# Kernel optimization log

Measured on AMD Instinct MI355X. Metric: run time of the kernel, lower is better.

The kernel has to match this reference:

```python
import jax, jax.numpy as jnp
import numpy as np
from jax import lax

B, H, W, CIN = 4, 64, 64, 1024
CMID = 512
NA = 9  # 3 sizes * 3 ratios
PRE_NMS, POST_NMS, IOU_THR = 6000, 300, 0.7  # eval-mode caps (training=False)


def setup_inputs() -> dict:
    key = jax.random.key(0)
    ks = jax.random.split(key, 4)
    feats = jax.random.normal(ks[0], (B, H, W, CIN), jnp.float32)
    # anchors: normalized ccwh (cx, cy, w, h) on a stride-16 grid of a 1024px image
    stride, img = 16.0, 1024.0
    cx = (jnp.arange(W, dtype=jnp.float32) + 0.5) * stride / img
    cy = (jnp.arange(H, dtype=jnp.float32) + 0.5) * stride / img
    sizes = jnp.array([64.0, 128.0, 256.0])
    ratios = jnp.array([0.5, 1.0, 2.0])
    ws = (sizes[:, None] * jnp.sqrt(ratios)[None, :]).reshape(-1) / img  # [9]
    hs = (sizes[:, None] / jnp.sqrt(ratios)[None, :]).reshape(-1) / img  # [9]
    cyg, cxg = jnp.meshgrid(cy, cx, indexing='ij')  # [H,W]
    ancs = jnp.stack([
        jnp.broadcast_to(cxg[:, :, None], (H, W, NA)),
        jnp.broadcast_to(cyg[:, :, None], (H, W, NA)),
        jnp.broadcast_to(ws[None, None, :], (H, W, NA)),
        jnp.broadcast_to(hs[None, None, :], (H, W, NA)),
    ], axis=-1)
    ancs = jnp.broadcast_to(ancs[None], (B, H, W, NA, 4)).astype(jnp.float32)
    ancs_valid = jnp.ones((B, H, W, NA), jnp.float32)
    w_bneck = jax.random.normal(ks[1], (CIN, CMID), jnp.float32) * 0.01
    b_bneck = jnp.zeros((CMID,), jnp.float32)
    w_cls = jax.random.normal(ks[2], (CMID, NA), jnp.float32) * 0.01
    b_cls = jnp.zeros((NA,), jnp.float32)
    w_reg = jax.random.normal(ks[3], (CMID, NA * 4), jnp.float32) * 0.01
    b_reg = jnp.zeros((NA * 4,), jnp.float32)
    return dict(feats=feats, ancs=ancs, ancs_valid=ancs_valid,
                w_bneck=w_bneck, b_bneck=b_bneck, w_cls=w_cls, b_cls=b_cls,
                w_reg=w_reg, b_reg=b_reg)


def _nms(boxes, max_out, thr):
    # boxes [N,4] xyxy, sorted by score descending. Greedy NMS via lax.scan.
    x1, y1, x2, y2 = boxes[:, 0], boxes[:, 1], boxes[:, 2], boxes[:, 3]
    areas = (x2 - x1) * (y2 - y1)

    def step(valid, _):
        idx = jnp.argmax(valid)  # first still-valid box = highest score
        has = valid[idx]
        b = boxes[idx]
        a = areas[idx]
        iw = jnp.maximum(jnp.minimum(b[2], x2) - jnp.maximum(b[0], x1), 0.0)
        ih = jnp.maximum(jnp.minimum(b[3], y2) - jnp.maximum(b[1], y1), 0.0)
        inter = iw * ih
        union = a + areas - inter
        iou = jnp.where(union > 0, inter / union, 0.0)
        keep = valid & (iou <= thr)
        keep = keep.at[idx].set(False)
        return jnp.where(has, keep, valid), jnp.where(has, idx, -1)

    _, sel = lax.scan(step, jnp.ones(boxes.shape[0], bool), None, length=max_out)
    return sel  # [max_out] selected indices, -1 = no more boxes


def _forward(feats, ancs, w_bneck, b_bneck, w_cls, b_cls, w_reg, b_reg):
    h = jax.nn.relu(jnp.einsum('bhwc,cm->bhwm', feats, w_bneck) + b_bneck)
    cls_pred = jax.nn.sigmoid(jnp.einsum('bhwm,mo->bhwo', h, w_cls) + b_cls)
    reg_pred = (jnp.einsum('bhwm,mo->bhwo', h, w_reg) + b_reg).reshape(B, H, W, NA, 4)
    cls_f = cls_pred.reshape(-1)
    reg_f = reg_pred.reshape(-1, 4)
    anc_f = ancs.reshape(-1, 4)
    # apply_offsets in ccwh: cx += tx*w, cy += ty*h, w *= exp(tw), h *= exp(th)
    cx = anc_f[:, 0] + reg_f[:, 0] * anc_f[:, 2]
    cy = anc_f[:, 1] + reg_f[:, 1] * anc_f[:, 3]
    ww = anc_f[:, 2] * jnp.exp(reg_f[:, 2])
    hh = anc_f[:, 3] * jnp.exp(reg_f[:, 3])
    # ccwh -> xyxy, clip to [0,1]
    boxes = jnp.stack([cx - ww / 2, cy - hh / 2, cx + ww / 2, cy + hh / 2], axis=-1)
    boxes = jnp.clip(boxes, 0.0, 1.0)
    order = jnp.argsort(-cls_f)[:PRE_NMS]
    boxes = boxes[order]
    sel = _nms(boxes, POST_NMS, IOU_THR)
    # pad unselected slots with zeros (TF returns a variable-length tensor)
    proposals = jnp.where(sel[:, None] >= 0, boxes[jnp.clip(sel, 0)], 0.0)
    return cls_pred, reg_pred, proposals


def reference(feats, ancs, ancs_valid, w_bneck, b_bneck, w_cls, b_cls, w_reg, b_reg):
    # ancs_valid is reshaped but never used in the original extract_proposals
    return _forward(feats, ancs, w_bneck, b_bneck, w_cls, b_cls, w_reg, b_reg)
```

## Files before the change

### kernel.cpp

```cpp
#include <hip/hip_runtime.h>
#include <cstdint>
#include <cstddef>

#define P_TOT    16384
#define CIN      1024
#define CMID     512
#define NA       9
#define NANC     147456
#define PRE_NMS  6000
#define POST_NMS 300
#define IOU_THR  0.7f
#define NWORDS   94
#define NHCOPY   4

#define CLS_OFF  0
#define REG_OFF  147456
#define PROP_OFF 737280

#define WS_H        0u
#define WS_MASK     0u
#define WS_HISTN    33554432u
#define WS_WCOMBT   34603008u
#define WS_BOXES    36700160u
#define WS_HIST     39059456u
#define WS_META     39321600u
#define WS_COLL     39321856u
#define WS_SBOX     39387392u
#define CAP_COLL    8192

__device__ __forceinline__ int imin(int a, int b) { return a < b ? a : b; }

__device__ __forceinline__ void gld_lds16f(const float* g, float* l) {
    __builtin_amdgcn_global_load_lds(
        (const __attribute__((address_space(1))) void*)g,
        (__attribute__((address_space(3))) void*)l,
        16, 0, 0);
}

__global__ __launch_bounds__(256)
__attribute__((amdgpu_waves_per_eu(1, 2)))
void gemm1_kernel(
    const float* __restrict__ A, const float* __restrict__ Bw,
    const float* __restrict__ bias, float* __restrict__ C,
    unsigned int* __restrict__ histN, unsigned int* __restrict__ meta,
    const float* __restrict__ wcls, const float* __restrict__ wreg,
    float* __restrict__ wcombT)
{
    __shared__ float As[2][16][132];
    __shared__ float Bs[2][16][128];

    const int t  = threadIdx.x;

    {
        const int fb = (int)blockIdx.x * 4 + (int)blockIdx.y;
        if (t < 128) {
            uint4* hz = (uint4*)histN;
            hz[fb * 128 + t] = make_uint4(0u, 0u, 0u, 0u);
        }
        if (fb == 0 && t < 64) meta[t] = 0u;
        if (t < 48) {
            float v = 0.f;
            if (t < 9)       v = wcls[fb * 9 + t];
            else if (t < 45) v = wreg[fb * 36 + (t - 9)];
            wcombT[t * CMID + fb] = v;
        }
    }

    const int m0 = blockIdx.x * 128;
    const int n0 = blockIdx.y * 128;
    const int tx = t & 15;
    const int ty = t >> 4;

    const int ar0 = t >> 2;
    const int ac0 = (t & 3) * 4;

    const float* asrc0 = A + (size_t)(m0 + ar0) * CIN + ac0;
    const float* asrc1 = asrc0 + (size_t)64 * CIN;
    const float* bsrc  = Bw + (size_t)(t >> 5) * CMID + n0 + (t & 31) * 4;
    float* bdst0 = &Bs[0][0][0] + t * 4;
    float* bdst1 = &Bs[1][0][0] + t * 4;

    float4 c0a{0,0,0,0}, c0b{0,0,0,0}, c1a{0,0,0,0}, c1b{0,0,0,0};
    float4 c2a{0,0,0,0}, c2b{0,0,0,0}, c3a{0,0,0,0}, c3b{0,0,0,0};
    float4 c4a{0,0,0,0}, c4b{0,0,0,0}, c5a{0,0,0,0}, c5b{0,0,0,0};
    float4 c6a{0,0,0,0}, c6b{0,0,0,0}, c7a{0,0,0,0}, c7b{0,0,0,0};

    gld_lds16f(bsrc, bdst0);
    gld_lds16f(bsrc + 8 * CMID, bdst0 + 1024);
    float4 pa0 = *(const float4*)(asrc0);
    float4 pa1 = *(const float4*)(asrc1);
    As[0][ac0 + 0][ar0] = pa0.x; As[0][ac0 + 1][ar0] = pa0.y;
    As[0][ac0 + 2][ar0] = pa0.z; As[0][ac0 + 3][ar0] = pa0.w;
    As[0][ac0 + 0][ar0 + 64] = pa1.x; As[0][ac0 + 1][ar0 + 64] = pa1.y;
    As[0][ac0 + 2][ar0 + 64] = pa1.z; As[0][ac0 + 3][ar0 + 64] = pa1.w;
    __syncthreads();

#define FMA4(acc, s, b) { acc.x += (s)*(b).x; acc.y += (s)*(b).y; \
                          acc.z += (s)*(b).z; acc.w += (s)*(b).w; }

    for (int kt = 0; kt < 64; ++kt) {
        const int cur = kt & 1, nxt = cur ^ 1;
        if (kt < 63) {
            const int k0 = (kt + 1) * 16;
            float* bd = nxt ? bdst1 : bdst0;
            gld_lds16f(bsrc + (size_t)k0 * CMID, bd);
            gld_lds16f(bsrc + (size_t)(k0 + 8) * CMID, bd + 1024);
            pa0 = *(const float4*)(asrc0 + k0);
            pa1 = *(const float4*)(asrc1 + k0);
        }
#pragma unroll 2
        for (int kk = 0; kk < 16; ++kk) {
            float4 a0 = *(const float4*)&As[cur][kk][ty * 4];
            float4 a1 = *(const float4*)&As[cur][kk][64 + ty * 4];
            float4 b0 = *(const float4*)&Bs[cur][kk][tx * 4];
            float4 b1 = *(const float4*)&Bs[cur][kk][64 + tx * 4];
            FMA4(c0a, a0.x, b0) FMA4(c0b, a0.x, b1)
            FMA4(c1a, a0.y, b0) FMA4(c1b, a0.y, b1)
            FMA4(c2a, a0.z, b0) FMA4(c2b, a0.z, b1)
            FMA4(c3a, a0.w, b0) FMA4(c3b, a0.w, b1)
            FMA4(c4a, a1.x, b0) FMA4(c4b, a1.x, b1)
            FMA4(c5a, a1.y, b0) FMA4(c5b, a1.y, b1)
            FMA4(c6a, a1.z, b0) FMA4(c6b, a1.z, b1)
            FMA4(c7a, a1.w, b0) FMA4(c7b, a1.w, b1)
        }
        if (kt < 63) {
            As[nxt][ac0 + 0][ar0] = pa0.x; As[nxt][ac0 + 1][ar0] = pa0.y;
            As[nxt][ac0 + 2][ar0] = pa0.z; As[nxt][ac0 + 3][ar0] = pa0.w;
            As[nxt][ac0 + 0][ar0 + 64] = pa1.x; As[nxt][ac0 + 1][ar0 + 64] = pa1.y;
            As[nxt][ac0 + 2][ar0 + 64] = pa1.z; As[nxt][ac0 + 3][ar0 + 64] = pa1.w;
        }
        __syncthreads();
    }
#undef FMA4

    const float4 bias0 = *(const float4*)(bias + n0 + tx * 4);
    const float4 bias1 = *(const float4*)(bias + n0 + 64 + tx * 4);
#define STROW(row, ca, cb) { \
    float4 o; \
    o.x = fmaxf(ca.x + bias0.x, 0.f); o.y = fmaxf(ca.y + bias0.y, 0.f); \
    o.z = fmaxf(ca.z + bias0.z, 0.f); o.w = fmaxf(ca.w + bias0.w, 0.f); \
    *(float4*)(C + (size_t)(row) * CMID + n0 + tx * 4) = o; \
    o.x = fmaxf(cb.x + bias1.x, 0.f); o.y = fmaxf(cb.y + bias1.y, 0.f); \
    o.z = fmaxf(cb.z + bias1.z, 0.f); o.w = fmaxf(cb.w + bias1.w, 0.f); \
    *(float4*)(C + (size_t)(row) * CMID + n0 + 64 + tx * 4) = o; }

    const int mr = m0 + ty * 4;
    STROW(mr + 0, c0a, c0b)   STROW(mr + 1, c1a, c1b)
    STROW(mr + 2, c2a, c2b)   STROW(mr + 3, c3a, c3b)
    STROW(mr + 64, c4a, c4b)  STROW(mr + 65, c5a, c5b)
    STROW(mr + 66, c6a, c6b)  STROW(mr + 67, c7a, c7b)
#undef STROW
}

__global__ __launch_bounds__(256) void gemm2_kernel(
    const float* __restrict__ h, const float* __restrict__ wcombT,
    const float* __restrict__ bcls, const float* __restrict__ breg,
    const float4* __restrict__ ancs, float* __restrict__ out,
    float4* __restrict__ boxes, unsigned int* __restrict__ histN)
{
    __shared__ float hS[32][68];
    __shared__ float wT[48][64];
    __shared__ float lt[32][49];

    const int t  = threadIdx.x;
    const int p0 = blockIdx.x * 32;
    const int px = t & 31;
    const int og = t >> 5;

    const int hr = t >> 3;
    const int hc = (t & 7) * 8;

    float acc[6] = {};

    for (int kt = 0; kt < 8; ++kt) {
        const int k0 = kt * 64;
        {
            const float* hp = h + (size_t)(p0 + hr) * CMID + k0 + hc;
            float4 v0 = *(const float4*)(hp);
            float4 v1 = *(const float4*)(hp + 4);
            *(float4*)&hS[hr][hc]     = v0;
            *(float4*)&hS[hr][hc + 4] = v1;
        }
        {
#pragma unroll
            for (int r = 0; r < 3; ++r) {
                int idx = t + r * 256;
                int row = idx >> 4, c4 = (idx & 15) * 4;
                *(float4*)&wT[row][c4] =
                    *(const float4*)&wcombT[(size_t)row * CMID + k0 + c4];
            }
        }
        __syncthreads();
#pragma unroll
        for (int q = 0; q < 16; ++q) {
            float4 hv4 = *(const float4*)&hS[px][q * 4];
            float4 w0 = *(const float4*)&wT[og * 6 + 0][q * 4];
            float4 w1 = *(const float4*)&wT[og * 6 + 1][q * 4];
            float4 w2 = *(const float4*)&wT[og * 6 + 2][q * 4];
            float4 w3 = *(const float4*)&wT[og * 6 + 3][q * 4];
            float4 w4 = *(const float4*)&wT[og * 6 + 4][q * 4];
            float4 w5 = *(const float4*)&wT[og * 6 + 5][q * 4];
            const float* hv = (const float*)&hv4;
            const float* p0w = (const float*)&w0;
            const float* p1w = (const float*)&w1;
            const float* p2w = (const float*)&w2;
            const float* p3w = (const float*)&w3;
            const float* p4w = (const float*)&w4;
            const float* p5w = (const float*)&w5;
#pragma unroll
            for (int j = 0; j < 4; ++j) {
                float hvj = hv[j];
                acc[0] += hvj * p0w[j];
                acc[1] += hvj * p1w[j];
                acc[2] += hvj * p2w[j];
                acc[3] += hvj * p3w[j];
                acc[4] += hvj * p4w[j];
                acc[5] += hvj * p5w[j];
            }
        }
        __syncthreads();
    }

#pragma unroll
    for (int c = 0; c < 6; ++c) {
        int o = og * 6 + c;
        float v = 0.f;
        if (o < 45) {
            float bv = (o < 9) ? bcls[o] : breg[o - 9];
            v = acc[c] + bv;
        }
        lt[px][o] = v;
    }
    __syncthreads();

#pragma unroll
    for (int rr = 0; rr < 2; ++rr) {
        int a_lin = t + rr * 256;
        if (a_lin < 288) {
            int px_l = a_lin / 9;
            int a    = a_lin - px_l * 9;
            int i    = (p0 + px_l) * 9 + a;

            float lg = lt[px_l][a];
            float score = 1.f / (1.f + expf(-lg));
            out[CLS_OFF + i] = score;

            float r0 = lt[px_l][9 + a * 4 + 0];
            float r1 = lt[px_l][9 + a * 4 + 1];
            float r2 = lt[px_l][9 + a * 4 + 2];
            float r3 = lt[px_l][9 + a * 4 + 3];
            float4 rg; rg.x = r0; rg.y = r1; rg.z = r2; rg.w = r3;
            *(float4*)(out + REG_OFF + (size_t)i * 4) = rg;

            float4 an = ancs[i];
            float cx = an.x + r0 * an.z;
            float cy = an.y + r1 * an.w;
            float ww = an.z * expf(r2);
            float hh = an.w * expf(r3);
            float4 bb;
            bb.x = fminf(fmaxf(cx - ww * 0.5f, 0.f), 1.f);
            bb.y = fminf(fmaxf(cy - hh * 0.5f, 0.f), 1.f);
            bb.z = fminf(fmaxf(cx + ww * 0.5f, 0.f), 1.f);
            bb.w = fminf(fmaxf(cy + hh * 0.5f, 0.f), 1.f);
            boxes[i] = bb;

            unsigned int sb = __float_as_uint(score);
            atomicAdd(&histN[(unsigned)(blockIdx.x & (NHCOPY - 1)) * 65536u + (sb >> 16)], 1u);
        }
    }
}

__global__ __launch_bounds__(256) void hreduce_kernel(
    const unsigned int* __restrict__ histN, unsigned int* __restrict__ hist)
{
    int b = blockIdx.x * 256 + threadIdx.x;
    unsigned int s = 0;
#pragma unroll
    for (int c = 0; c < NHCOPY; ++c) s += histN[(unsigned)c * 65536u + b];
    hist[b] = s;
}

__global__ __launch_bounds__(256) void scan_kernel(
    const unsigned int* __restrict__ hist, unsigned int* __restrict__ meta)
{
    __shared__ unsigned int sums[256];
    __shared__ unsigned int sc[256];
    __shared__ unsigned int sc2[256];
    __shared__ int cstar;
    __shared__ unsigned int saShared;
    __shared__ int tbin;

    int t = threadIdx.x;
    if (t == 0) tbin = -1;

    unsigned int s = 0;
    int base = t << 8;
    for (int b = 0; b < 256; b += 4) {
        uint4 v = *(const uint4*)(hist + base + b);
        s += v.x + v.y + v.z + v.w;
    }
    sums[t] = s;
    __syncthreads();

    sc[t] = sums[255 - t];
    __syncthreads();
    for (int off = 1; off < 256; off <<= 1) {
        unsigned int v = sc[t];
        unsigned int add = (t >= off) ? sc[t - off] : 0u;
        __syncthreads();
        sc[t] = v + add;
        __syncthreads();
    }
    {
        unsigned int sa = (t == 255) ? 0u : sc[254 - t];
        if (sa < PRE_NMS && sa + sums[t] >= PRE_NMS) { cstar = t; saShared = sa; }
    }
    __syncthreads();

    int c = cstar;
    unsigned int SA = saShared;
    sc2[t] = hist[c * 256 + 255 - t];
    __syncthreads();
    for (int off = 1; off < 256; off <<= 1) {
        unsigned int v = sc2[t];
        unsigned int add = (t >= off) ? sc2[t - off] : 0u;
        __syncthreads();
        sc2[t] = v + add;
        __syncthreads();
    }
    {
        unsigned int si = sc2[255 - t];
        int cand = (SA + si >= PRE_NMS) ? t : -1;
        atomicMax(&tbin, cand);
    }
    __syncthreads();
    if (t == 0) meta[1] = (unsigned int)(c * 256 + tbin);
}

__global__ __launch_bounds__(256) void collect_kernel(
    const float* __restrict__ scores, const unsigned int* __restrict__ meta,
    unsigned long long* __restrict__ coll, unsigned int* __restrict__ cnt)
{
    int i = blockIdx.x * 256 + threadIdx.x;
    unsigned int T = meta[1];
    unsigned int sb = __float_as_uint(scores[i]);
    if ((sb >> 16) >= T) {
        unsigned int pos = atomicAdd(cnt, 1u);
        if (pos < CAP_COLL)
            coll[pos] = ((unsigned long long)sb << 32) |
                        (unsigned long long)(0xFFFFFFFFu - (unsigned int)i);
    }
}

__global__ __launch_bounds__(256) void rank_kernel(
    const unsigned long long* __restrict__ coll,
    const unsigned int* __restrict__ cnt,
    const float4* __restrict__ boxes, float4* __restrict__ sboxes)
{
    const int t = threadIdx.x;
    const int lane = t & 63;
    const int gwave = blockIdx.x * 4 + (t >> 6);
    unsigned int n = cnt[0];
    if (n > CAP_COLL) n = CAP_COLL;
    if (gwave * 16 >= (int)n) return;

    unsigned long long me[16];
    int rank[16];
#pragma unroll
    for (int i = 0; i < 16; ++i) {
        int mi = gwave * 16 + i;
        me[i] = (mi < (int)n) ? coll[mi] : ~0ULL;
        rank[i] = 0;
    }

    for (int j = 0; j < CAP_COLL; j += 64) {
        unsigned long long k = ((unsigned)(j + lane) < n) ? coll[j + lane] : 0ULL;
#pragma unroll
        for (int i = 0; i < 16; ++i)
            rank[i] += (int)__popcll(__ballot(k > me[i]));
    }

#pragma unroll
    for (int i = 0; i < 16; ++i) {
        int mi = gwave * 16 + i;
        if (mi < (int)n && rank[i] < PRE_NMS && lane == i) {
            unsigned int idx = 0xFFFFFFFFu - (unsigned int)(me[i] & 0xFFFFFFFFULL);
            if (idx > NANC - 1) idx = NANC - 1;
            sboxes[rank[i]] = boxes[idx];
        }
    }
}

__global__ __launch_bounds__(64) void nmsmat_kernel(
    const float4* __restrict__ sboxes, unsigned long long* __restrict__ mask)
{
    const int rb = blockIdx.x, cb = blockIdx.y;
    if (cb < rb) return;
    __shared__ float cx1[64], cy1[64], cx2[64], cy2[64], car[64];

    const int t = threadIdx.x;
    const int c = cb * 64 + t;
    float4 b = (c < PRE_NMS) ? sboxes[c] : make_float4(0.f, 0.f, 0.f, 0.f);
    cx1[t] = b.x; cy1[t] = b.y; cx2[t] = b.z; cy2[t] = b.w;
    car[t] = (b.z - b.x) * (b.w - b.y);
    __syncthreads();

    const int r = rb * 64 + t;
    if (r >= PRE_NMS) return;
    const float4 rbx = sboxes[r];
    const float ra = (rbx.z - rbx.x) * (rbx.w - rbx.y);

    unsigned long long w = 0ULL;
#pragma unroll 8
    for (int i = 0; i < 64; ++i) {
        int j = cb * 64 + i;
        float iw = fmaxf(fminf(rbx.z, cx2[i]) - fmaxf(rbx.x, cx1[i]), 0.f);
        float ih = fmaxf(fminf(rbx.w, cy2[i]) - fmaxf(rbx.y, cy1[i]), 0.f);
        float inter = iw * ih;
        float uni = ra + car[i] - inter;
        float iou = (uni > 0.f) ? (inter / uni) : 0.f;
        if (iou > IOU_THR && j > r) w |= (1ULL << i);
    }
    mask[(size_t)r * NWORDS + cb] = w;
}

__global__ __launch_bounds__(64) void nmsresolve_kernel(
    const float4* __restrict__ sboxes,
    const unsigned long long* __restrict__ mask,
    float* __restrict__ prop)
{
    __shared__ unsigned long long rowbuf[64 * NWORDS];
    __shared__ int picks[POST_NMS];

    const int t = threadIdx.x;
    for (int j = t; j < POST_NMS * 4; j += 64) prop[j] = 0.f;

    const int w0 = 2 * t, w1 = 2 * t + 1;
    unsigned long long s0 = 0ULL, s1 = 0ULL;
    int cnt = 0;

    for (int c = 0; c < NWORDS && cnt < POST_NMS; ++c) {
        unsigned long long aw = __shfl((c & 1) ? s1 : s0, c >> 1, 64);
        unsigned long long valid = ~aw;
        if (c == 93) valid &= (1ULL << 48) - 1ULL;
        if (!valid) continue;

        {
            const float* src = (const float*)(mask + (size_t)c * 64 * NWORDS) + t * 4;
            float* dst = (float*)&rowbuf[0] + t * 4;
#pragma unroll
            for (int k = 0; k < 47; ++k)
                gld_lds16f(src + k * 256, dst + k * 256);
        }
        asm volatile("s_waitcnt vmcnt(0)" ::: "memory");
        __builtin_amdgcn_sched_barrier(0);

        while (valid && cnt < POST_NMS) {
            const int b = __builtin_ctzll(valid);
            if (t == 0) picks[cnt] = c * 64 + b;
            ++cnt;

            unsigned long long rx = 0ULL, ry = 0ULL;
            if (t < 47) {
                ulonglong2 rr = *(const ulonglong2*)&rowbuf[(size_t)b * NWORDS + 2 * t];
                rx = rr.x; ry = rr.y;
            }
            unsigned long long m0 = (w0 >= c) ? rx : 0ULL;
            unsigned long long m1 = (w1 >= c) ? ry : 0ULL;
            s0 |= m0; s1 |= m1;
            if (w0 == c) s0 |= (1ULL << b);
            if (w1 == c) s1 |= (1ULL << b);

            unsigned long long wc = __shfl((c & 1) ? m1 : m0, c >> 1, 64);
            valid &= ~wc;
            valid &= ~(1ULL << b);
        }
    }

    __syncthreads();

    for (int i = t; i < cnt; i += 64) {
        float4 bb = sboxes[picks[i]];
        *(float4*)(prop + i * 4) = bb;
    }
}

extern "C" void kernel_launch(void* const* d_in, const int* in_sizes, int n_in,
                              void* d_out, int out_size, void* d_ws, size_t ws_size,
                              hipStream_t stream)
{
    const float*  feats   = (const float*)d_in[0];
    const float4* ancs    = (const float4*)d_in[1];
    const float*  w_bneck = (const float*)d_in[3];
    const float*  b_bneck = (const float*)d_in[4];
    const float*  w_cls   = (const float*)d_in[5];
    const float*  b_cls   = (const float*)d_in[6];
    const float*  w_reg   = (const float*)d_in[7];
    const float*  b_reg   = (const float*)d_in[8];

    float* out = (float*)d_out;
    char*  ws  = (char*)d_ws;
    float*              h      = (float*)(ws + WS_H);
    float4*             boxes  = (float4*)(ws + WS_BOXES);
    unsigned int*       histN  = (unsigned int*)(ws + WS_HISTN);
    unsigned int*       hist   = (unsigned int*)(ws + WS_HIST);
    float*              wcombT = (float*)(ws + WS_WCOMBT);
    unsigned int*       meta   = (unsigned int*)(ws + WS_META);
    unsigned long long* coll   = (unsigned long long*)(ws + WS_COLL);
    float4*             sboxes = (float4*)(ws + WS_SBOX);
    unsigned long long* mask   = (unsigned long long*)(ws + WS_MASK);

    gemm1_kernel<<<dim3(128, 4), 256, 0, stream>>>(feats, w_bneck, b_bneck, h,
                                                   histN, meta,
                                                   w_cls, w_reg, wcombT);
    gemm2_kernel<<<512, 256, 0, stream>>>(h, wcombT, b_cls, b_reg,
                                          ancs, out, boxes, histN);
    hreduce_kernel<<<256, 256, 0, stream>>>(histN, hist);
    scan_kernel<<<1, 256, 0, stream>>>(hist, meta);
    collect_kernel<<<576, 256, 0, stream>>>(out, meta, coll, &meta[0]);
    rank_kernel<<<128, 256, 0, stream>>>(coll, meta, boxes, sboxes);
    nmsmat_kernel<<<dim3(94, 94), 64, 0, stream>>>(sboxes, mask);
    nmsresolve_kernel<<<1, 64, 0, stream>>>(sboxes, mask, out + PROP_OFF);
}
```

Measured before the change: 587.4 us.

## Double-buffer NMS mask chunk loads and skip fully suppressed chunks

The NMS resolve kernel now prefetches the next 64-row mask chunk into a second LDS buffer while the current chunk is processed. It uses ballots over the suppression state to jump directly to the next chunk that still holds a valid box, restaging the buffer when the jump is not to the prefetched chunk. This hides global-to-LDS latency on the serial NMS path at the cost of doubled LDS use. The gemm2 weight tile is also padded from 64 to 68 columns, likely to reduce LDS bank conflicts.

```diff
diff --git a/kernel.cpp b/kernel.cpp
--- a/kernel.cpp
+++ b/kernel.cpp
@@ -159,7 +159,7 @@
     float4* __restrict__ boxes, unsigned int* __restrict__ histN)
 {
     __shared__ float hS[32][68];
-    __shared__ float wT[48][64];
+    __shared__ float wT[48][68];
     __shared__ float lt[32][49];
 
     const int t  = threadIdx.x;
@@ -429,7 +429,7 @@
     const unsigned long long* __restrict__ mask,
     float* __restrict__ prop)
 {
-    __shared__ unsigned long long rowbuf[64 * NWORDS];
+    __shared__ unsigned long long rowbuf[2][64 * NWORDS];
     __shared__ int picks[POST_NMS];
 
     const int t = threadIdx.x;
@@ -439,21 +439,26 @@
     unsigned long long s0 = 0ULL, s1 = 0ULL;
     int cnt = 0;
 
-    for (int c = 0; c < NWORDS && cnt < POST_NMS; ++c) {
+#define STAGE_CH(cc, buf) { \
+    const float* src = (const float*)(mask + (size_t)(cc) * 64 * NWORDS) + t * 4; \
+    float* dst = (float*)&rowbuf[buf][0] + t * 4; \
+    _Pragma("unroll") \
+    for (int k = 0; k < 47; ++k) gld_lds16f(src + k * 256, dst + k * 256); }
+
+    STAGE_CH(0, 0)
+    int c = 0, cur = 0;
+
+    while (c < NWORDS && cnt < POST_NMS) {
+        const int cn = c + 1;
+        const bool pf = (cn < NWORDS);
+        if (pf) { STAGE_CH(cn, cur ^ 1) }
+        if (pf) asm volatile("s_waitcnt vmcnt(47)" ::: "memory");
+        else    asm volatile("s_waitcnt vmcnt(0)"  ::: "memory");
+        __builtin_amdgcn_sched_barrier(0);
+
         unsigned long long aw = __shfl((c & 1) ? s1 : s0, c >> 1, 64);
         unsigned long long valid = ~aw;
         if (c == 93) valid &= (1ULL << 48) - 1ULL;
-        if (!valid) continue;
-
-        {
-            const float* src = (const float*)(mask + (size_t)c * 64 * NWORDS) + t * 4;
-            float* dst = (float*)&rowbuf[0] + t * 4;
-#pragma unroll
-            for (int k = 0; k < 47; ++k)
-                gld_lds16f(src + k * 256, dst + k * 256);
-        }
-        asm volatile("s_waitcnt vmcnt(0)" ::: "memory");
-        __builtin_amdgcn_sched_barrier(0);
 
         while (valid && cnt < POST_NMS) {
             const int b = __builtin_ctzll(valid);
@@ -462,7 +467,7 @@
 
             unsigned long long rx = 0ULL, ry = 0ULL;
             if (t < 47) {
-                ulonglong2 rr = *(const ulonglong2*)&rowbuf[(size_t)b * NWORDS + 2 * t];
+                ulonglong2 rr = *(const ulonglong2*)&rowbuf[cur][(size_t)b * NWORDS + 2 * t];
                 rx = rr.x; ry = rr.y;
             }
             unsigned long long m0 = (w0 >= c) ? rx : 0ULL;
@@ -475,7 +480,33 @@
             valid &= ~wc;
             valid &= ~(1ULL << b);
         }
-    }
+        if (cnt >= POST_NMS) break;
+
+        unsigned long long v0m = ~s0, v1m = ~s1;
+        if (w1 == 93) v1m &= (1ULL << 48) - 1ULL;
+        if (w0 >= 94) v0m = 0ULL;
+        if (w1 >= 94) v1m = 0ULL;
+        unsigned long long em = __ballot(v0m != 0ULL);
+        unsigned long long om = __ballot(v1m != 0ULL);
+        const int te = (c + 2) >> 1;
+        const int to = (c + 1) >> 1;
+        unsigned long long emh = (te < 64) ? (em >> te) : 0ULL;
+        unsigned long long omh = (to < 64) ? (om >> to) : 0ULL;
+        int we = emh ? 2 * (te + (int)__builtin_ctzll(emh))     : 0x7fffffff;
+        int wo = omh ? 2 * (to + (int)__builtin_ctzll(omh)) + 1 : 0x7fffffff;
+        int c2 = we < wo ? we : wo;
+        if (c2 >= NWORDS) break;
+
+        if (pf && c2 == cn) {
+            c = c2; cur ^= 1;
+        } else {
+            asm volatile("s_waitcnt vmcnt(0)" ::: "memory");
+            __builtin_amdgcn_sched_barrier(0);
+            STAGE_CH(c2, cur ^ 1)
+            c = c2; cur ^= 1;
+        }
+    }
+#undef STAGE_CH
 
     __syncthreads();
 
```

Result: no change. 587.6 us (+0.0%).
